# Performance work log

Hardware: AMD Instinct MI355X
Metric: run time of the kernel (lower is better)

Reference implementation:

```python
import jax, jax.numpy as jnp
import numpy as np
from jax import lax

SIM_THRESHOLD = 0.8
EPS = 1e-12  # torch F.normalize clamp_min eps


def _l2norm(x):
    # faithful to F.normalize(p=2, dim=1): divide by max(||x||, eps)
    n = jnp.sqrt(jnp.sum(x * x, axis=1, keepdims=True))
    return x / jnp.maximum(n, EPS)


def setup_inputs() -> dict:
    key = jax.random.key(0)
    k1, k2, k3, k4, k5 = jax.random.split(key, 5)
    return {
        "query_features": jax.random.normal(k1, (2048, 256), dtype=jnp.float32),
        "memory_keys": jax.random.normal(k2, (100000, 256), dtype=jnp.float32),
        "memory_values": jax.random.randint(k3, (100000,), 0, 1000, dtype=jnp.int64)
        if jax.config.jax_enable_x64
        else jax.random.randint(k3, (100000,), 0, 1000, dtype=jnp.int32),
        "upd_features": jax.random.normal(k4, (128, 256), dtype=jnp.float32),
        "upd_labels": jax.random.randint(k5, (128,), 0, 1000, dtype=jnp.int32),
    }


def reference(query_features, memory_keys, memory_values, upd_features, upd_labels):
    # ---- retrieve(): normalize + matmul + row-max + label gather ----
    qn = _l2norm(query_features)                      # [Q, D]
    mn = _l2norm(memory_keys)                         # [M, D]
    sims = jnp.einsum("qd,md->qm", qn, mn)            # [Q, M]
    conf = jnp.max(sims, axis=1)                      # [Q]
    idx = jnp.argmax(sims, axis=1)                    # [Q]
    retrieved = memory_values[idx]                    # [Q]

    # ---- update() (memory full): threshold-gated masked-argmin scatter ----
    # Torch code computes memory_normalized / memory_values copies ONCE before
    # the loop, so all similarities/class masks use the ORIGINAL memory; only
    un = _l2norm(upd_features)                        # [B, D]
    usims = jnp.einsum("bd,md->bm", un, mn)           # [B, M]
    max_sim = jnp.max(usims, axis=1)                  # [B]
    do_update = max_sim < SIM_THRESHOLD               # [B]
    same_class = memory_values[None, :] == upd_labels[:, None]  # [B, M]
    has_same = jnp.any(same_class, axis=1)
    masked = jnp.where(same_class, usims, jnp.inf)
    tgt = jnp.where(has_same, jnp.argmin(masked, axis=1), jnp.argmin(usims, axis=1))

    def step(carry, x):
        keys, vals = carry
        t, feat, lab, do = x
        keys = keys.at[t].set(jnp.where(do, feat, keys[t]))
        vals = vals.at[t].set(jnp.where(do, lab.astype(vals.dtype), vals[t]))
        return (keys, vals), None

    (new_keys, new_vals), _ = lax.scan(
        step, (memory_keys, memory_values), (tgt, upd_features, upd_labels, do_update)
    )
    return retrieved, conf, new_keys, new_vals
```

## Files before the change

### kernel.cpp

```cpp
#include <hip/hip_runtime.h>

typedef _Float16 half8 __attribute__((ext_vector_type(8)));
typedef __fp16 fp16x2 __attribute__((ext_vector_type(2)));
typedef float floatx4 __attribute__((ext_vector_type(4)));
typedef float f4v __attribute__((ext_vector_type(4)));
typedef unsigned long long ull;


__device__ __forceinline__ unsigned fmap(float f) {
    unsigned u = __float_as_uint(f);
    return (u & 0x80000000u) ? ~u : (u | 0x80000000u);
}
__device__ __forceinline__ float funmap(unsigned m) {
    unsigned u = (m & 0x80000000u) ? (m & 0x7FFFFFFFu) : ~m;
    return __uint_as_float(u);
}

__device__ __forceinline__ half8 nt_load_h8(const half8* p) {
    return __builtin_nontemporal_load(p);
}
__device__ __forceinline__ f4v nt_load_f4(const f4v* p) {
    return __builtin_nontemporal_load(p);
}
__device__ __forceinline__ void nt_store_h8(half8 v, half8* p) {
    __builtin_nontemporal_store(v, p);
}
__device__ __forceinline__ void nt_store_f4(f4v v, f4v* p) {
    __builtin_nontemporal_store(v, p);
}

__device__ __forceinline__ void split8n(const f4v& v0, const f4v& v1, float rn_,
                                        half8& h, half8& l) {
    float s[8];
    #pragma unroll
    for (int j = 0; j < 4; ++j) { s[j] = v0[j] * rn_; s[4 + j] = v1[j] * rn_; }
    #pragma unroll
    for (int j = 0; j < 8; j += 2) {
        fp16x2 hh = __builtin_amdgcn_cvt_pkrtz(s[j], s[j + 1]);
        h[j] = (_Float16)hh[0]; h[j + 1] = (_Float16)hh[1];
        float r0 = (s[j]     - (float)hh[0]) * 2048.0f;
        float r1 = (s[j + 1] - (float)hh[1]) * 2048.0f;
        fp16x2 ll = __builtin_amdgcn_cvt_pkrtz(r0, r1);
        l[j] = (_Float16)ll[0]; l[j + 1] = (_Float16)ll[1];
    }
}

__device__ __forceinline__ void split8r(const f4v& v0, const f4v& v1,
                                        half8& h, half8& l) {
    #pragma unroll
    for (int j = 0; j < 4; j += 2) {
        fp16x2 hh = __builtin_amdgcn_cvt_pkrtz(v0[j], v0[j + 1]);
        h[j] = (_Float16)hh[0]; h[j + 1] = (_Float16)hh[1];
        float r0 = (v0[j]     - (float)hh[0]) * 2048.0f;
        float r1 = (v0[j + 1] - (float)hh[1]) * 2048.0f;
        fp16x2 ll = __builtin_amdgcn_cvt_pkrtz(r0, r1);
        l[j] = (_Float16)ll[0]; l[j + 1] = (_Float16)ll[1];
    }
    #pragma unroll
    for (int j = 0; j < 4; j += 2) {
        fp16x2 hh = __builtin_amdgcn_cvt_pkrtz(v1[j], v1[j + 1]);
        h[4 + j] = (_Float16)hh[0]; h[4 + j + 1] = (_Float16)hh[1];
        float r0 = (v1[j]     - (float)hh[0]) * 2048.0f;
        float r1 = (v1[j + 1] - (float)hh[1]) * 2048.0f;
        fp16x2 ll = __builtin_amdgcn_cvt_pkrtz(r0, r1);
        l[4 + j] = (_Float16)ll[0]; l[4 + j + 1] = (_Float16)ll[1];
    }
}


__global__ void init_kernel(ull* packed, unsigned* maxsim,
                            ull* minall, ull* minsame, int Q, int Bn) {
    int i = blockIdx.x * blockDim.x + threadIdx.x;
    if (i < Q) packed[i] = 0ULL;
    if (i < Bn) { maxsim[i] = 0u; minall[i] = ~0ULL; minsame[i] = ~0ULL; }
}

__global__ void norms_kernel(const float* __restrict__ X, float* __restrict__ rn, int rows) {
    int w = (blockIdx.x * blockDim.x + threadIdx.x) >> 6;
    int lane = threadIdx.x & 63;
    if (w >= rows) return;
    float4 v = *(const float4*)&X[(long)w * 256 + lane * 4];
    float s = v.x * v.x + v.y * v.y + v.z * v.z + v.w * v.w;
    #pragma unroll
    for (int o = 32; o >= 1; o >>= 1) s += __shfl_xor(s, o, 64);
    if (lane == 0) rn[w] = 1.0f / fmaxf(sqrtf(s), 1e-12f);
}

__global__ __launch_bounds__(256) void prep_b(const float* __restrict__ mk,
                                              _Float16* __restrict__ Bh,
                                              _Float16* __restrict__ Bl, int M) {
    __shared__ float tile[16][272];
    __shared__ float rns[16];
    const int mt = blockIdx.x;
    const int m0 = mt << 4;
    const int t = threadIdx.x;

    #pragma unroll
    for (int i = 0; i < 4; ++i) {
        int flat = i * 256 + t;
        int row = flat >> 6;
        int c4 = (flat & 63) << 2;
        f4v f = (f4v){0.f, 0.f, 0.f, 0.f};
        if (m0 + row < M) f = nt_load_f4((const f4v*)&mk[((long)(m0 + row)) * 256 + c4]);
        *(f4v*)&tile[row][c4] = f;
    }
    __syncthreads();

    const int wave = t >> 6, lane = t & 63;
    #pragma unroll
    for (int rr = 0; rr < 4; ++rr) {
        int row = wave * 4 + rr;
        f4v v = *(f4v*)&tile[row][lane << 2];
        float s = v.x * v.x + v.y * v.y + v.z * v.z + v.w * v.w;
        #pragma unroll
        for (int o = 32; o >= 1; o >>= 1) s += __shfl_xor(s, o, 64);
        if (lane == 0) rns[row] = 1.0f / fmaxf(sqrtf(s), 1e-12f);
    }
    __syncthreads();

    #pragma unroll
    for (int i = 0; i < 2; ++i) {
        int fi = i * 256 + t;
        int kc = fi >> 6;
        int fl = fi & 63;
        int r = fl & 15, sub = fl >> 4;
        int k0 = (kc << 5) + (sub << 3);
        float rn = rns[r];
        f4v v0 = *(f4v*)&tile[r][k0];
        f4v v1 = *(f4v*)&tile[r][k0 + 4];
        half8 h, l;
        split8n(v0, v1, rn, h, l);
        long idx = ((long)mt * 8 + kc) * 64 + fl;
        nt_store_h8(h, ((half8*)Bh) + idx);
        nt_store_h8(l, ((half8*)Bl) + idx);
    }
}


__global__ __launch_bounds__(512, 4) void retrieve_fused(
    const float* __restrict__ qf, const float* __restrict__ uf,
    const half8* __restrict__ Bh, const half8* __restrict__ Bl,
    const int* __restrict__ mv, const int* __restrict__ lbl,
    ull* __restrict__ packed, unsigned* __restrict__ maxsim,
    ull* __restrict__ minall, ull* __restrict__ minsame,
    int M, int Mtiles, int Q, int Bn) {
    __shared__ half8 AhL[2][512];
    __shared__ half8 AlL[2][512];

    const int tid = threadIdx.x;
    const int wave = tid >> 6, lane = tid & 63;
    const int mset = blockIdx.x >> 1;
    const int half = blockIdx.x & 1;
    const int tmt = mset * 8 + wave;
    const bool valid = tmt < Mtiles;
    const int m0w = valid ? tmt * 16 + (lane & 15) : 0;

    half8 bhr[8], blr[8];
    #pragma unroll
    for (int kc = 0; kc < 8; ++kc) {
        if (valid) {
            bhr[kc] = nt_load_h8(&Bh[((long)tmt * 8 + kc) * 64 + lane]);
            blr[kc] = nt_load_h8(&Bl[((long)tmt * 8 + kc) * 64 + lane]);
        } else {
            bhr[kc] = (half8){0, 0, 0, 0, 0, 0, 0, 0};
            blr[kc] = (half8){0, 0, 0, 0, 0, 0, 0, 0};
        }
    }
    const int mvv = valid ? mv[m0w] : -2;
    const unsigned lowbits = ~(unsigned)m0w;

    const int QT = Q >> 4;
    const int NT = QT + (Bn >> 4);

    const int start = half ? (NT >> 1) : 0;
    const int end   = half ? NT : (NT >> 1);
    const int len   = end - start;

    auto stage = [&](int b, int qt) {
        int kc = tid >> 6;
        int fl = tid & 63;
        int row = qt * 16 + (fl & 15);
        const float* src = (row < Q) ? &qf[(long)row * 256]
                                     : &uf[(long)(row - Q) * 256];
        int k0 = (kc << 5) + ((fl >> 4) << 3);
        f4v v0 = *(const f4v*)(src + k0);
        f4v v1 = *(const f4v*)(src + k0 + 4);
        half8 h, l;
        split8r(v0, v1, h, l);
        AhL[b][kc * 64 + fl] = h;
        AlL[b][kc * 64 + fl] = l;
    };

    const int g4 = ((lane >> 4) << 2);
    int qt = start + (mset % len);
    stage(0, qt);
    int buf = 0;

    #pragma unroll 1
    for (int ii = 0; ii < len; ++ii) {
        int qtn = qt + 1; if (qtn == end) qtn = start;
        __syncthreads();
        if (ii + 1 < len) stage(buf ^ 1, qtn);

        floatx4 accH  = (floatx4){0.f, 0.f, 0.f, 0.f};
        floatx4 accMa = (floatx4){0.f, 0.f, 0.f, 0.f};
        floatx4 accMb = (floatx4){0.f, 0.f, 0.f, 0.f};
        #pragma unroll
        for (int kc = 0; kc < 8; ++kc) {
            half8 ah = AhL[buf][kc * 64 + lane];
            half8 al = AlL[buf][kc * 64 + lane];
            accH  = __builtin_amdgcn_mfma_f32_16x16x32_f16(ah, bhr[kc], accH,  0, 0, 0);
            accMa = __builtin_amdgcn_mfma_f32_16x16x32_f16(ah, blr[kc], accMa, 0, 0, 0);
            accMb = __builtin_amdgcn_mfma_f32_16x16x32_f16(al, bhr[kc], accMb, 0, 0, 0);
        }
        buf ^= 1;

        if (valid) {
            if (qt < QT) {
                int qb = (qt << 4) + g4;
                #pragma unroll
                for (int r = 0; r < 4; ++r) {
                    float s = accH[r] + (accMa[r] + accMb[r]) * (1.0f / 2048.0f);
                    ull key = (((ull)fmap(s)) << 32) | lowbits;
                    if (key > packed[qb + r]) atomicMax(&packed[qb + r], key);
                }
            } else {
                int ub = ((qt - QT) << 4) + g4;
                #pragma unroll
                for (int r = 0; r < 4; ++r) {
                    float s = accH[r] + (accMa[r] + accMb[r]) * (1.0f / 2048.0f);
                    unsigned ms = fmap(s);
                    ull key = (((ull)ms) << 32) | (unsigned)m0w;
                    int lb = lbl[ub + r];
                    if (ms > maxsim[ub + r]) atomicMax(&maxsim[ub + r], ms);
                    if (key < minall[ub + r]) atomicMin(&minall[ub + r], key);
                    if (lb == mvv && key < minsame[ub + r]) atomicMin(&minsame[ub + r], key);
                }
            }
        }
        qt = qtn;
    }
}


__global__ void finish_retrieve(const ull* __restrict__ packed,
                                const int* __restrict__ memvals,
                                const float* __restrict__ rq,
                                float* __restrict__ out, int Q) {
    int q = blockIdx.x * blockDim.x + threadIdx.x;
    if (q >= Q) return;
    ull key = packed[q];
    unsigned m = ~((unsigned)(key & 0xFFFFFFFFu));
    float conf = funmap((unsigned)(key >> 32)) * rq[q];
    out[q] = (float)memvals[m];
    out[Q + q] = conf;
}

__global__ void finish_upd(const unsigned* __restrict__ maxsim,
                           const ull* __restrict__ minall,
                           const ull* __restrict__ minsame,
                           const float* __restrict__ ru,
                           int* __restrict__ wtgt, int Bn) {
    __shared__ int tg[256];
    __shared__ unsigned char du[256];
    int b = threadIdx.x;
    int t = -1; bool d = false;
    if (b < Bn) {
        d = funmap(maxsim[b]) * ru[b] < 0.8f;
        ull ks = minsame[b];
        ull ka = minall[b];
        t = (ks != ~0ULL) ? (int)(ks & 0xFFFFFFFFu) : (int)(ka & 0xFFFFFFFFu);
        tg[b] = t; du[b] = d ? 1 : 0;
    }
    __syncthreads();
    if (b < Bn) {
        bool win = d;
        if (win)
            for (int b2 = b + 1; b2 < Bn; ++b2)
                if (du[b2] && tg[b2] == t) { win = false; break; }
        wtgt[b] = win ? t : -1;
    }
}

__global__ void copy_keys(const f4v* __restrict__ src, f4v* __restrict__ dst, long n4) {
    long i = blockIdx.x * (long)blockDim.x + threadIdx.x;
    long stride = (long)gridDim.x * blockDim.x;
    for (; i < n4; i += stride) nt_store_f4(nt_load_f4(&src[i]), &dst[i]);
}

__global__ void copy_vals(const int* __restrict__ src, float* __restrict__ dst, int n) {
    int i = blockIdx.x * blockDim.x + threadIdx.x;
    if (i < n) dst[i] = (float)src[i];
}

__global__ void scatter_kernel(const int* __restrict__ wtgt, const float4* __restrict__ upd4,
                               const int* __restrict__ lbl, float4* __restrict__ keys4,
                               float* __restrict__ vals) {
    int b = blockIdx.x;
    int t = wtgt[b];
    if (t < 0) return;
    int l = threadIdx.x;
    keys4[(long)t * 64 + l] = upd4[(long)b * 64 + l];
    if (l == 0) vals[t] = (float)lbl[b];
}


extern "C" void kernel_launch(void* const* d_in, const int* in_sizes, int n_in,
                              void* d_out, int out_size, void* d_ws, size_t ws_size,
                              hipStream_t stream) {
    const float* qf = (const float*)d_in[0];
    const float* mk = (const float*)d_in[1];
    const int*   mv = (const int*)d_in[2];
    const float* uf = (const float*)d_in[3];
    const int*   ul = (const int*)d_in[4];

    const int D = 256;
    const int Q = in_sizes[0] / D;
    const int M = in_sizes[2];
    const int Bn = in_sizes[3] / D;

    float* out = (float*)d_out;
    float* out_keys = out + 2 * (long)Q;
    float* out_vals = out_keys + (long)M * D;

    _Float16* Bh = (_Float16*)out_keys;
    _Float16* Bl = Bh + (size_t)M * D;

    char* ov = (char*)out_vals;
    ull* packed      = (ull*)(ov);
    ull* minall      = (ull*)(ov + 16384);
    ull* minsame     = (ull*)(ov + 17408);
    unsigned* maxsim = (unsigned*)(ov + 18432);
    float* rq        = (float*)(ov + 18944);
    float* ru        = (float*)(ov + 27136);

    int* wtgt = (int*)d_ws;

    const int Mtiles = (M + 15) / 16;
    const int msets = (Mtiles + 7) / 8;
    const int grid_g = msets * 2;

    int initN = (Q > Bn ? Q : Bn);
    init_kernel<<<(initN + 255) / 256, 256, 0, stream>>>(packed, maxsim, minall, minsame, Q, Bn);

    norms_kernel<<<(Q + 3) / 4, 256, 0, stream>>>(qf, rq, Q);
    norms_kernel<<<(Bn + 3) / 4, 256, 0, stream>>>(uf, ru, Bn);

    prep_b<<<Mtiles, 256, 0, stream>>>(mk, Bh, Bl, M);

    retrieve_fused<<<grid_g, 512, 0, stream>>>(
        qf, uf, (const half8*)Bh, (const half8*)Bl, mv, ul,
        packed, maxsim, minall, minsame, M, Mtiles, Q, Bn);

    finish_retrieve<<<(Q + 255) / 256, 256, 0, stream>>>(packed, mv, rq, out, Q);
    finish_upd<<<1, Bn, 0, stream>>>(maxsim, minall, minsame, ru, wtgt, Bn);

    copy_keys<<<2048, 256, 0, stream>>>((const f4v*)mk, (f4v*)out_keys, (long)M * (D / 4));
    copy_vals<<<(M + 255) / 256, 256, 0, stream>>>(mv, out_vals, M);
    scatter_kernel<<<Bn, 64, 0, stream>>>(wtgt, (const float4*)uf, ul, (float4*)out_keys, out_vals);
}
```

Before: 663.5 us.

## Process two memory tiles per wave to reuse staged query fragments

Each wave now keeps B fragments for two 16-row memory tiles in registers and runs MFMAs for both against every staged query tile. The number of blocks is halved, so staging LDS traffic and fp32-to-fp16 splitting of query rows are amortized over twice as many memory rows. The atomic reduction also reads the current value once per row and shares it between both tiles. Launch bounds drop to 2 blocks per CU to fit the doubled register footprint, which lowers occupancy.

```diff
diff --git a/kernel.cpp b/kernel.cpp
--- a/kernel.cpp
+++ b/kernel.cpp
@@ -137,7 +137,7 @@
 }
 
 
-__global__ __launch_bounds__(512, 4) void retrieve_fused(
+__global__ __launch_bounds__(512, 2) void retrieve_fused(
     const float* __restrict__ qf, const float* __restrict__ uf,
     const half8* __restrict__ Bh, const half8* __restrict__ Bl,
     const int* __restrict__ mv, const int* __restrict__ lbl,
@@ -151,23 +151,35 @@
     const int wave = tid >> 6, lane = tid & 63;
     const int mset = blockIdx.x >> 1;
     const int half = blockIdx.x & 1;
-    const int tmt = mset * 8 + wave;
-    const bool valid = tmt < Mtiles;
-    const int m0w = valid ? tmt * 16 + (lane & 15) : 0;
-
-    half8 bhr[8], blr[8];
+    const int tmt0 = (mset * 8 + wave) * 2;
+    const int tmt1 = tmt0 + 1;
+    const bool valid0 = tmt0 < Mtiles;
+    const bool valid1 = tmt1 < Mtiles;
+    const int m0w0 = valid0 ? tmt0 * 16 + (lane & 15) : 0;
+    const int m0w1 = valid1 ? tmt1 * 16 + (lane & 15) : 0;
+
+    half8 bhr[2][8], blr[2][8];
     #pragma unroll
     for (int kc = 0; kc < 8; ++kc) {
-        if (valid) {
-            bhr[kc] = nt_load_h8(&Bh[((long)tmt * 8 + kc) * 64 + lane]);
-            blr[kc] = nt_load_h8(&Bl[((long)tmt * 8 + kc) * 64 + lane]);
+        if (valid0) {
+            bhr[0][kc] = nt_load_h8(&Bh[((long)tmt0 * 8 + kc) * 64 + lane]);
+            blr[0][kc] = nt_load_h8(&Bl[((long)tmt0 * 8 + kc) * 64 + lane]);
         } else {
-            bhr[kc] = (half8){0, 0, 0, 0, 0, 0, 0, 0};
-            blr[kc] = (half8){0, 0, 0, 0, 0, 0, 0, 0};
-        }
-    }
-    const int mvv = valid ? mv[m0w] : -2;
-    const unsigned lowbits = ~(unsigned)m0w;
+            bhr[0][kc] = (half8){0, 0, 0, 0, 0, 0, 0, 0};
+            blr[0][kc] = (half8){0, 0, 0, 0, 0, 0, 0, 0};
+        }
+        if (valid1) {
+            bhr[1][kc] = nt_load_h8(&Bh[((long)tmt1 * 8 + kc) * 64 + lane]);
+            blr[1][kc] = nt_load_h8(&Bl[((long)tmt1 * 8 + kc) * 64 + lane]);
+        } else {
+            bhr[1][kc] = (half8){0, 0, 0, 0, 0, 0, 0, 0};
+            blr[1][kc] = (half8){0, 0, 0, 0, 0, 0, 0, 0};
+        }
+    }
+    const int mvv0 = valid0 ? mv[m0w0] : -2;
+    const int mvv1 = valid1 ? mv[m0w1] : -2;
+    const unsigned lowbits0 = ~(unsigned)m0w0;
+    const unsigned lowbits1 = ~(unsigned)m0w1;
 
     const int QT = Q >> 4;
     const int NT = QT + (Bn >> 4);
@@ -202,39 +214,65 @@
         __syncthreads();
         if (ii + 1 < len) stage(buf ^ 1, qtn);
 
-        floatx4 accH  = (floatx4){0.f, 0.f, 0.f, 0.f};
-        floatx4 accMa = (floatx4){0.f, 0.f, 0.f, 0.f};
-        floatx4 accMb = (floatx4){0.f, 0.f, 0.f, 0.f};
+        floatx4 accH[2], accMa[2], accMb[2];
+        #pragma unroll
+        for (int t = 0; t < 2; ++t) {
+            accH[t]  = (floatx4){0.f, 0.f, 0.f, 0.f};
+            accMa[t] = (floatx4){0.f, 0.f, 0.f, 0.f};
+            accMb[t] = (floatx4){0.f, 0.f, 0.f, 0.f};
+        }
         #pragma unroll
         for (int kc = 0; kc < 8; ++kc) {
             half8 ah = AhL[buf][kc * 64 + lane];
             half8 al = AlL[buf][kc * 64 + lane];
-            accH  = __builtin_amdgcn_mfma_f32_16x16x32_f16(ah, bhr[kc], accH,  0, 0, 0);
-            accMa = __builtin_amdgcn_mfma_f32_16x16x32_f16(ah, blr[kc], accMa, 0, 0, 0);
-            accMb = __builtin_amdgcn_mfma_f32_16x16x32_f16(al, bhr[kc], accMb, 0, 0, 0);
+            #pragma unroll
+            for (int t = 0; t < 2; ++t) {
+                accH[t]  = __builtin_amdgcn_mfma_f32_16x16x32_f16(ah, bhr[t][kc], accH[t],  0, 0, 0);
+                accMa[t] = __builtin_amdgcn_mfma_f32_16x16x32_f16(ah, blr[t][kc], accMa[t], 0, 0, 0);
+                accMb[t] = __builtin_amdgcn_mfma_f32_16x16x32_f16(al, bhr[t][kc], accMb[t], 0, 0, 0);
+            }
         }
         buf ^= 1;
 
-        if (valid) {
-            if (qt < QT) {
-                int qb = (qt << 4) + g4;
-                #pragma unroll
-                for (int r = 0; r < 4; ++r) {
-                    float s = accH[r] + (accMa[r] + accMb[r]) * (1.0f / 2048.0f);
-                    ull key = (((ull)fmap(s)) << 32) | lowbits;
-                    if (key > packed[qb + r]) atomicMax(&packed[qb + r], key);
+        if (qt < QT) {
+            int qb = (qt << 4) + g4;
+            #pragma unroll
+            for (int r = 0; r < 4; ++r) {
+                ull cur = packed[qb + r];
+                if (valid0) {
+                    float s = accH[0][r] + (accMa[0][r] + accMb[0][r]) * (1.0f / 2048.0f);
+                    ull key = (((ull)fmap(s)) << 32) | lowbits0;
+                    if (key > cur) atomicMax(&packed[qb + r], key);
                 }
-            } else {
-                int ub = ((qt - QT) << 4) + g4;
-                #pragma unroll
-                for (int r = 0; r < 4; ++r) {
-                    float s = accH[r] + (accMa[r] + accMb[r]) * (1.0f / 2048.0f);
+                if (valid1) {
+                    float s = accH[1][r] + (accMa[1][r] + accMb[1][r]) * (1.0f / 2048.0f);
+                    ull key = (((ull)fmap(s)) << 32) | lowbits1;
+                    if (key > cur) atomicMax(&packed[qb + r], key);
+                }
+            }
+        } else {
+            int ub = ((qt - QT) << 4) + g4;
+            #pragma unroll
+            for (int r = 0; r < 4; ++r) {
+                unsigned curm = maxsim[ub + r];
+                ull cura = minall[ub + r];
+                ull curs = minsame[ub + r];
+                int lb = lbl[ub + r];
+                if (valid0) {
+                    float s = accH[0][r] + (accMa[0][r] + accMb[0][r]) * (1.0f / 2048.0f);
                     unsigned ms = fmap(s);
-                    ull key = (((ull)ms) << 32) | (unsigned)m0w;
-                    int lb = lbl[ub + r];
-                    if (ms > maxsim[ub + r]) atomicMax(&maxsim[ub + r], ms);
-                    if (key < minall[ub + r]) atomicMin(&minall[ub + r], key);
-                    if (lb == mvv && key < minsame[ub + r]) atomicMin(&minsame[ub + r], key);
+                    ull key = (((ull)ms) << 32) | (unsigned)m0w0;
+                    if (ms > curm) atomicMax(&maxsim[ub + r], ms);
+                    if (key < cura) atomicMin(&minall[ub + r], key);
+                    if (lb == mvv0 && key < curs) atomicMin(&minsame[ub + r], key);
+                }
+                if (valid1) {
+                    float s = accH[1][r] + (accMa[1][r] + accMb[1][r]) * (1.0f / 2048.0f);
+                    unsigned ms = fmap(s);
+                    ull key = (((ull)ms) << 32) | (unsigned)m0w1;
+                    if (ms > curm) atomicMax(&maxsim[ub + r], ms);
+                    if (key < cura) atomicMin(&minall[ub + r], key);
+                    if (lb == mvv1 && key < curs) atomicMin(&minsame[ub + r], key);
                 }
             }
         }
@@ -337,7 +375,7 @@
     int* wtgt = (int*)d_ws;
 
     const int Mtiles = (M + 15) / 16;
-    const int msets = (Mtiles + 7) / 8;
+    const int msets = (Mtiles + 15) / 16;
     const int grid_g = msets * 2;
 
     int initN = (Q > Bn ? Q : Bn);
```

Measured after the change: 724.8 us. 1.09x slower.
